# Kernel tuning notes

Hardware: AMD Instinct MI355X
Metric: run time of the kernel (lower is better)

Reference implementation:

```python
import jax, jax.numpy as jnp
import numpy as np

HEADS = 16
PHI = (1.0 + np.sqrt(5.0)) / 2.0


def setup_inputs() -> dict:
    key = jax.random.key(0)
    k1, k2, k3, k4 = jax.random.split(key, 4)
    B, L, D = 2, 2048, 1024
    x = jax.random.normal(k1, (B, L, D), dtype=jnp.float32)
    # nn.Linear(dim, 3*dim, bias=False): store as [D, 3D] for x @ W
    w_qkv = jax.random.normal(k2, (D, 3 * D), dtype=jnp.float32) * (D ** -0.5)
    w_proj = jax.random.normal(k3, (D, D), dtype=jnp.float32) * (D ** -0.5)
    b_proj = jax.random.normal(k4, (D,), dtype=jnp.float32) * 0.01
    return {"x": x, "w_qkv": w_qkv, "w_proj": w_proj, "b_proj": b_proj}


def phi_bias(L):
    # pos[i] = (i * phi) mod 1 ; bias = log(exp(-|pos_i - pos_j|) + 1e-8)
    pos = (jnp.arange(L, dtype=jnp.float32) * PHI) % 1.0
    dist = jnp.abs(pos[:, None] - pos[None, :])  # [L, L]
    return jnp.log(jnp.exp(-dist) + 1e-8)


def reference(x, w_qkv, w_proj, b_proj):
    B, L, D = x.shape
    H = HEADS
    Dh = D // H
    scale = Dh ** -0.5
    qkv = (x @ w_qkv).reshape(B, L, 3, H, Dh)
    q = jnp.transpose(qkv[:, :, 0], (0, 2, 1, 3))  # [B, H, L, Dh]
    k = jnp.transpose(qkv[:, :, 1], (0, 2, 1, 3))
    v = jnp.transpose(qkv[:, :, 2], (0, 2, 1, 3))
    attn = jnp.einsum("bhid,bhjd->bhij", q, k) * scale  # [B, H, L, L]
    attn = attn + phi_bias(L)[None, None]  # additive phi-distance bias
    attn = jax.nn.softmax(attn, axis=-1)
    out = jnp.einsum("bhij,bhjd->bhid", attn, v)  # [B, H, L, Dh]
    out = jnp.transpose(out, (0, 2, 1, 3)).reshape(B, L, D)
    return out @ w_proj + b_proj
```

## Files before the change

### kernel.cpp

```cpp
#include <hip/hip_runtime.h>
#include <math.h>


typedef _Float16 f16;
typedef _Float16 f16x4 __attribute__((ext_vector_type(4)));
typedef _Float16 f16x8 __attribute__((ext_vector_type(8)));
typedef float f32x4 __attribute__((ext_vector_type(4)));

#define MFMA32(a, b, c) __builtin_amdgcn_mfma_f32_16x16x32_f16(a, b, c, 0, 0, 0)

static constexpr int Bsz = 2, Lseq = 2048, Dm = 1024, H = 16, Dh = 64;
static constexpr int Mtot = Bsz * Lseq;
static constexpr int NQKV = 3 * Dm;
static constexpr float PHI_F = 1.61803398874989484820f;
static constexpr float LOG2E = 1.44269504088896f;
static constexpr float QS = 0.125f * LOG2E;
static constexpr float CSTEP = 0.55417527999932633f;

__device__ __forceinline__ void load16_to_lds(const f16* g, f16* l) {
  __builtin_amdgcn_global_load_lds(
      (const __attribute__((address_space(1))) unsigned int*)g,
      (__attribute__((address_space(3))) unsigned int*)l, 16, 0, 0);
}

__device__ __forceinline__ void barrier_fenced() {
  __builtin_amdgcn_sched_barrier(0);
  __builtin_amdgcn_s_barrier();
  __builtin_amdgcn_sched_barrier(0);
}

__global__ __launch_bounds__(256) void prep_fused(
    const float* __restrict__ x, f16* __restrict__ xb,
    const float* __restrict__ wqkv, f16* __restrict__ wqkvT,
    const float* __restrict__ wproj, f16* __restrict__ wpT) {
  __shared__ float tile[32][33];
  int blk = blockIdx.x;
  if (blk < 4096) {
    int i = (blk * 256 + threadIdx.x) * 4;
    float4 v = *reinterpret_cast<const float4*>(x + i);
    f16 t[4] = {(f16)v.x, (f16)v.y, (f16)v.z, (f16)v.w};
    *reinterpret_cast<uint2*>(xb + i) = *reinterpret_cast<uint2*>(t);
    return;
  }
  const float* in;
  f16* out;
  int N, bx, by;
  if (blk < 7168) {
    int local = blk - 4096;
    bx = local % 96; by = local / 96; N = NQKV;
    in = wqkv; out = wqkvT;
  } else {
    int local = blk - 7168;
    bx = local & 31; by = local >> 5; N = Dm;
    in = wproj; out = wpT;
  }
  int n0 = bx * 32, k0 = by * 32;
  int tx = threadIdx.x & 31, ty = threadIdx.x >> 5;
#pragma unroll
  for (int r = 0; r < 32; r += 8)
    tile[ty + r][tx] = in[(size_t)(k0 + ty + r) * N + n0 + tx];
  __syncthreads();
#pragma unroll
  for (int r = 0; r < 32; r += 8)
    out[(size_t)(n0 + ty + r) * Dm + k0 + tx] = (f16)tile[tx][ty + r];
}

__global__ __launch_bounds__(512, 1) void gemm_qkv(
    const f16* __restrict__ A, const f16* __restrict__ Bt,
    f16* __restrict__ qb, f16* __restrict__ kb, f16* __restrict__ vb) {
  __shared__ f16 As[2 * 256 * 64];
  __shared__ f16 Bs[2 * 192 * 64];

  int tid = threadIdx.x;
  int wave = tid >> 6, lane = tid & 63;
  int quad = lane >> 4, l16 = lane & 15;
  int warp_m = wave >> 2, warp_n = wave & 3;
  int wm = warp_m * 128, wn = warp_n * 48;

  int lid = blockIdx.x;
  int xcd = lid & 7, t = lid >> 3;
  int mg = xcd & 3, ng = xcd >> 2;
  int m0 = (mg * 4 + (t >> 3)) * 256;
  int n0 = (ng * 8 + (t & 7)) * 192;

  const int gu = (lane & 7) ^ (lane >> 3);
  const f16* gAb = A + (size_t)(m0 + wave * 8 + (lane >> 3)) * Dm + gu * 8;
  const f16* gBb = Bt + (size_t)(n0 + wave * 8 + (lane >> 3)) * Dm + gu * 8;

  auto stageA = [&](int buf, int h, int kn) __attribute__((always_inline)) {
#pragma unroll
    for (int i = 0; i < 2; i++)
      load16_to_lds(gAb + (size_t)(h * 128 + i * 64) * Dm + kn,
                    As + buf * 16384 + (h * 128 + i * 64 + wave * 8) * 64);
  };
  auto stageB = [&](int buf, int part, int kn) __attribute__((always_inline)) {
    if (part == 0) {
#pragma unroll
      for (int i = 0; i < 2; i++)
        load16_to_lds(gBb + (size_t)(i * 64) * Dm + kn,
                      Bs + buf * 12288 + (i * 64 + wave * 8) * 64);
    } else {
      load16_to_lds(gBb + (size_t)128 * Dm + kn,
                    Bs + buf * 12288 + (128 + wave * 8) * 64);
    }
  };

  f32x4 acc[8][3] = {};

  auto do_tile = [&](int buf, int t_) __attribute__((always_inline)) {
    const f16* Ab = As + buf * 16384 + (wm + l16) * 64;
    const f16* Bb = Bs + buf * 12288 + (wn + l16) * 64;
    int nbuf = buf ^ 1;
    int kA = ((t_ + 1) & 15) * 64;
    int kB = ((t_ + 2) & 15) * 64;

    f16x8 a[4][2], b0[2][2], b1[2];

#pragma unroll
    for (int m = 0; m < 4; m++)
#pragma unroll
      for (int s = 0; s < 2; s++)
        a[m][s] = *reinterpret_cast<const f16x8*>(
            Ab + m * 16 * 64 + (((s * 4 + quad) ^ (l16 & 7)) * 8));
#pragma unroll
    for (int n = 0; n < 2; n++)
#pragma unroll
      for (int s = 0; s < 2; s++)
        b0[n][s] = *reinterpret_cast<const f16x8*>(
            Bb + n * 16 * 64 + (((s * 4 + quad) ^ (l16 & 7)) * 8));
    stageA(nbuf, 0, kA);
    barrier_fenced();
    asm volatile("s_waitcnt lgkmcnt(0)" ::: "memory");
    __builtin_amdgcn_sched_barrier(0);
    __builtin_amdgcn_s_setprio(1);
#pragma unroll
    for (int m = 0; m < 4; m++)
#pragma unroll
      for (int n = 0; n < 2; n++) {
        acc[m][n] = MFMA32(a[m][0], b0[n][0], acc[m][n]);
        acc[m][n] = MFMA32(a[m][1], b0[n][1], acc[m][n]);
      }
    __builtin_amdgcn_s_setprio(0);
    barrier_fenced();

#pragma unroll
    for (int s = 0; s < 2; s++)
      b1[s] = *reinterpret_cast<const f16x8*>(
          Bb + 2 * 16 * 64 + (((s * 4 + quad) ^ (l16 & 7)) * 8));
    stageA(nbuf, 1, kA);
    barrier_fenced();
    asm volatile("s_waitcnt lgkmcnt(0)" ::: "memory");
    __builtin_amdgcn_sched_barrier(0);
    __builtin_amdgcn_s_setprio(1);
#pragma unroll
    for (int m = 0; m < 4; m++) {
      acc[m][2] = MFMA32(a[m][0], b1[0], acc[m][2]);
      acc[m][2] = MFMA32(a[m][1], b1[1], acc[m][2]);
    }
    __builtin_amdgcn_s_setprio(0);
    barrier_fenced();

#pragma unroll
    for (int m = 0; m < 4; m++)
#pragma unroll
      for (int s = 0; s < 2; s++)
        a[m][s] = *reinterpret_cast<const f16x8*>(
            Ab + (4 + m) * 16 * 64 + (((s * 4 + quad) ^ (l16 & 7)) * 8));
    stageB(buf, 0, kB);
    barrier_fenced();
    asm volatile("s_waitcnt lgkmcnt(0)" ::: "memory");
    __builtin_amdgcn_sched_barrier(0);
    __builtin_amdgcn_s_setprio(1);
#pragma unroll
    for (int m = 0; m < 4; m++)
#pragma unroll
      for (int n = 0; n < 2; n++) {
        acc[4 + m][n] = MFMA32(a[m][0], b0[n][0], acc[4 + m][n]);
        acc[4 + m][n] = MFMA32(a[m][1], b0[n][1], acc[4 + m][n]);
      }
    __builtin_amdgcn_s_setprio(0);
    barrier_fenced();

    stageB(buf, 1, kB);
    asm volatile("s_waitcnt vmcnt(3)" ::: "memory");
    barrier_fenced();
    __builtin_amdgcn_s_setprio(1);
#pragma unroll
    for (int m = 0; m < 4; m++) {
      acc[4 + m][2] = MFMA32(a[m][0], b1[0], acc[4 + m][2]);
      acc[4 + m][2] = MFMA32(a[m][1], b1[1], acc[4 + m][2]);
    }
    __builtin_amdgcn_s_setprio(0);
    barrier_fenced();
  };

  stageA(0, 0, 0);
  stageA(0, 1, 0);
  stageB(0, 0, 0);
  stageB(0, 1, 0);
  stageB(1, 0, 64);
  stageB(1, 1, 64);
  asm volatile("s_waitcnt vmcnt(3)" ::: "memory");
  barrier_fenced();

#pragma unroll 1
  for (int tt = 0; tt < 16; tt += 2) {
    do_tile(0, tt);
    do_tile(1, tt + 1);
  }
  asm volatile("s_waitcnt vmcnt(0)" ::: "memory");

#pragma unroll
  for (int i = 0; i < 8; i++) {
#pragma unroll
    for (int j = 0; j < 3; j++) {
      int n = n0 + wn + j * 16 + l16;
      int ty = n >> 10;
      int df = n & 1023;
      int h = df >> 6, dh = df & 63;
      int mb = m0 + wm + i * 16 + quad * 4;
      int b = mb >> 11, l = mb & 2047;
      int bhh = b * H + h;
      if (ty == 2) {
        int jj = l & 63;
        int jh = jj >> 5, rem = jj & 31;
        int qd = (rem & 15) >> 2;
        int e0 = (rem >= 16) ? 4 : 0;
        f16x4 tmp;
#pragma unroll
        for (int r = 0; r < 4; r++) tmp[r] = (f16)acc[i][j][r];
        *reinterpret_cast<uint2*>(
            vb + (size_t)bhh * (Dh * Lseq) + (l >> 6) * 4096 + dh * 64 +
            (jh * 4 + qd) * 8 + e0) = *reinterpret_cast<uint2*>(&tmp);
      } else {
        size_t idx = (((size_t)bhh) * Lseq + l) * Dh + dh;
        if (ty == 0) {
#pragma unroll
          for (int r = 0; r < 4; r++)
            qb[idx + (size_t)r * Dh] = (f16)(acc[i][j][r] * QS);
        } else {
#pragma unroll
          for (int r = 0; r < 4; r++)
            kb[idx + (size_t)r * Dh] = (f16)acc[i][j][r];
        }
      }
    }
  }
}

__global__ __launch_bounds__(256) void gemm_proj(
    const f16* __restrict__ A, const f16* __restrict__ Bt,
    float* __restrict__ out, const float* __restrict__ bias) {
  constexpr int MI = 4, AI = 4;
  __shared__ f16 As[2 * 128 * 64];
  __shared__ f16 Bs[2 * 128 * 64];

  int tid = threadIdx.x;
  int wave = tid >> 6, lane = tid & 63;
  int quad = lane >> 4, l16 = lane & 15;
  int wm = (wave >> 1) * 64, wn = (wave & 1) * 64;

  int lid = blockIdx.x;
  int xcd = lid & 7, t = lid >> 3;
  int m0 = (xcd * 4 + (t >> 3)) * 128;
  int n0 = (t & 7) * 128;

  const int gu = (lane & 7) ^ (lane >> 3);
  const f16* gA[AI];
  f16* lA[AI];
#pragma unroll
  for (int i = 0; i < AI; i++) {
    int it = wave * AI + i;
    gA[i] = A + (size_t)(m0 + it * 8 + (lane >> 3)) * Dm + gu * 8;
    lA[i] = As + it * 512;
  }
  const f16* gB[4];
  f16* lB[4];
#pragma unroll
  for (int i = 0; i < 4; i++) {
    int it = wave * 4 + i;
    gB[i] = Bt + (size_t)(n0 + it * 8 + (lane >> 3)) * Dm + gu * 8;
    lB[i] = Bs + it * 512;
  }

  auto stage = [&](int buf, int k0) __attribute__((always_inline)) {
#pragma unroll
    for (int i = 0; i < AI; i++) load16_to_lds(gA[i] + k0, lA[i] + buf * 8192);
#pragma unroll
    for (int i = 0; i < 4; i++) load16_to_lds(gB[i] + k0, lB[i] + buf * 8192);
  };

  f32x4 acc[MI][4] = {};

  stage(0, 0);
  asm volatile("s_waitcnt vmcnt(0)" ::: "memory");
  barrier_fenced();

#pragma unroll 1
  for (int kt = 0; kt < 16; kt++) {
    int buf = kt & 1;
    const f16* Ab = As + buf * 8192;
    const f16* Bb = Bs + buf * 8192;

    f16x8 a[2][MI], b[2][4];
#pragma unroll
    for (int s = 0; s < 2; s++) {
#pragma unroll
      for (int i = 0; i < MI; i++) {
        int row = wm + i * 16 + l16;
        a[s][i] = *reinterpret_cast<const f16x8*>(
            Ab + row * 64 + (((s * 4 + quad) ^ (l16 & 7)) * 8));
      }
#pragma unroll
      for (int j = 0; j < 4; j++) {
        int row = wn + j * 16 + l16;
        b[s][j] = *reinterpret_cast<const f16x8*>(
            Bb + row * 64 + (((s * 4 + quad) ^ (l16 & 7)) * 8));
      }
    }

    int kn = (kt + 1 < 16) ? (kt + 1) * 64 : 0;
    stage(buf ^ 1, kn);

    __builtin_amdgcn_s_setprio(1);
#pragma unroll
    for (int s = 0; s < 2; s++)
#pragma unroll
      for (int i = 0; i < MI; i++)
#pragma unroll
        for (int j = 0; j < 4; j++)
          acc[i][j] = MFMA32(a[s][i], b[s][j], acc[i][j]);
    __builtin_amdgcn_s_setprio(0);

    asm volatile("s_waitcnt vmcnt(0)" ::: "memory");
    barrier_fenced();
  }

#pragma unroll
  for (int i = 0; i < MI; i++)
#pragma unroll
    for (int j = 0; j < 4; j++) {
      int n = n0 + wn + j * 16 + l16;
#pragma unroll
      for (int r = 0; r < 4; r++) {
        int m = m0 + wm + i * 16 + quad * 4 + r;
        out[(size_t)m * Dm + n] = acc[i][j][r] + bias[n];
      }
    }
}

__global__ __launch_bounds__(512, 4) void attn_kernel(
    const f16* __restrict__ qb,
    const f16* __restrict__ kb,
    const f16* __restrict__ vb,
    f16* __restrict__ ctx) {
  __shared__ __align__(16) unsigned char smem[33280];
  f16* Ks = (f16*)smem;
  f16* Vs = (f16*)(smem + 8192);

  int id = blockIdx.x;
  int bh = (id & 7) * 4 + ((id >> 3) >> 4);
  int q0 = ((id >> 3) & 15) * 128;

  int tid = threadIdx.x, wave = tid >> 6, lane = tid & 63;
  int quad = lane >> 4, l16 = lane & 15;
  int jhalf = wave >> 2, qq = wave & 3;

  f16x8 qfrag[2][2];
  float pq[2];
#pragma unroll
  for (int set = 0; set < 2; set++) {
    int q = q0 + qq * 32 + set * 16 + l16;
    const f16* Qrow = qb + ((size_t)bh * Lseq + q) * Dh;
    qfrag[set][0] = *reinterpret_cast<const f16x8*>(Qrow + quad * 8);
    qfrag[set][1] = *reinterpret_cast<const f16x8*>(Qrow + 32 + quad * 8);
    pq[set] = fmodf((float)q * PHI_F, 1.0f);
  }

  float pk[2][4];
#pragma unroll
  for (int jb = 0; jb < 2; jb++)
#pragma unroll
    for (int r = 0; r < 4; r++) {
      int j = jhalf * 32 + jb * 16 + quad * 4 + r;
      pk[jb][r] = fmodf((float)j * PHI_F, 1.0f);
    }

  const f16* Kbh = kb + (size_t)bh * Lseq * Dh;
  const f16* Vbh = vb + (size_t)bh * Dh * Lseq;
  const int gu = (lane & 7) ^ (lane >> 3);
  int g8 = wave * 8 + (lane >> 3);
  const f16* gK = Kbh + (size_t)g8 * Dh + gu * 8;
  const f16* gV = Vbh + (size_t)g8 * 64 + gu * 8;
  f16* lK = Ks + wave * 512;
  f16* lV = Vs + wave * 512;

  const f16 one = (f16)1.0f;
  const f16x8 ones8 = {one, one, one, one, one, one, one, one};

  f32x4 acc_o[2][4] = {};
  f32x4 acc_l[2] = {};

  for (int j0 = 0; j0 < Lseq; j0 += 64) {
    __syncthreads();
    load16_to_lds(gK + (size_t)j0 * Dh, lK);
    load16_to_lds(gV + (size_t)j0 * 64, lV);
    __syncthreads();

    f32x4 accs[2][2] = {};
    __builtin_amdgcn_s_setprio(1);
#pragma unroll
    for (int s = 0; s < 2; s++)
#pragma unroll
      for (int jb = 0; jb < 2; jb++) {
        f16x8 kf = *reinterpret_cast<const f16x8*>(
            Ks + (jhalf * 32 + jb * 16 + l16) * 64 + (((s * 4 + quad) ^ (l16 & 7)) * 8));
        accs[0][jb] = MFMA32(kf, qfrag[0][s], accs[0][jb]);
        accs[1][jb] = MFMA32(kf, qfrag[1][s], accs[1][jb]);
      }
    __builtin_amdgcn_s_setprio(0);

    f16x8 pf8[2];
#pragma unroll
    for (int set = 0; set < 2; set++) {
#pragma unroll
      for (int jb = 0; jb < 2; jb++) {
        float p[4];
#pragma unroll
        for (int r = 0; r < 4; r++) {
          float d = pq[set] - pk[jb][r];
          float arg = fmaf(-LOG2E, fabsf(d), accs[set][jb][r]);
          p[r] = __builtin_amdgcn_exp2f(arg);
        }
        auto lo = __builtin_amdgcn_cvt_pkrtz(p[0], p[1]);
        auto hi = __builtin_amdgcn_cvt_pkrtz(p[2], p[3]);
        pf8[set][jb * 4 + 0] = lo[0];
        pf8[set][jb * 4 + 1] = lo[1];
        pf8[set][jb * 4 + 2] = hi[0];
        pf8[set][jb * 4 + 3] = hi[1];
      }
      acc_l[set] = MFMA32(ones8, pf8[set], acc_l[set]);
    }
#pragma unroll
    for (int jb = 0; jb < 2; jb++)
#pragma unroll
      for (int r = 0; r < 4; r++)
        pk[jb][r] = __builtin_amdgcn_fractf(pk[jb][r] + CSTEP);

    __builtin_amdgcn_s_setprio(1);
#pragma unroll
    for (int dblk = 0; dblk < 4; dblk++) {
      int row = dblk * 16 + l16;
      f16x8 va = *reinterpret_cast<const f16x8*>(
          Vs + row * 64 + (((jhalf * 4 + quad) ^ (l16 & 7)) * 8));
      acc_o[0][dblk] = MFMA32(va, pf8[0], acc_o[0][dblk]);
      acc_o[1][dblk] = MFMA32(va, pf8[1], acc_o[1][dblk]);
    }
    __builtin_amdgcn_s_setprio(0);
  }

  __syncthreads();
  float* Oex = (float*)smem;
  float* Lex = (float*)(smem + 32768);
  if (jhalf == 1) {
#pragma unroll
    for (int set = 0; set < 2; set++) {
#pragma unroll
      for (int dblk = 0; dblk < 4; dblk++)
#pragma unroll
        for (int r = 0; r < 4; r++)
          Oex[(((qq * 2 + set) * 4 + dblk) * 16 + quad * 4 + r) * 16 + l16] =
              acc_o[set][dblk][r];
      if (quad == 0) Lex[(qq * 2 + set) * 16 + l16] = acc_l[set][0];
    }
  }
  __syncthreads();
  if (jhalf == 0) {
    int b = bh >> 4, h = bh & 15;
#pragma unroll
    for (int set = 0; set < 2; set++) {
      float ltot = acc_l[set][0] + Lex[(qq * 2 + set) * 16 + l16];
      float inv = 1.0f / ltot;
      int q = q0 + qq * 32 + set * 16 + l16;
      f16* crow = ctx + (size_t)(b * Lseq + q) * Dm + h * 64;
#pragma unroll
      for (int dblk = 0; dblk < 4; dblk++) {
        f16x4 o;
#pragma unroll
        for (int r = 0; r < 4; r++) {
          float full = acc_o[set][dblk][r] +
              Oex[(((qq * 2 + set) * 4 + dblk) * 16 + quad * 4 + r) * 16 + l16];
          o[r] = (f16)(full * inv);
        }
        *reinterpret_cast<uint2*>(crow + dblk * 16 + quad * 4) =
            *reinterpret_cast<uint2*>(&o);
      }
    }
  }
}

extern "C" void kernel_launch(void* const* d_in, const int* in_sizes, int n_in,
                              void* d_out, int out_size, void* d_ws, size_t ws_size,
                              hipStream_t stream) {
  const float* x      = (const float*)d_in[0];
  const float* w_qkv  = (const float*)d_in[1];
  const float* w_proj = (const float*)d_in[2];
  const float* b_proj = (const float*)d_in[3];
  float* out = (float*)d_out;

  f16* xb    = (f16*)d_ws;
  f16* wqkvT = xb + (size_t)Mtot * Dm;
  f16* wpT   = wqkvT + (size_t)NQKV * Dm;
  f16* qb    = wpT + (size_t)Dm * Dm;
  f16* kb    = qb + (size_t)Bsz * H * Lseq * Dh;
  f16* vb    = kb + (size_t)Bsz * H * Lseq * Dh;
  f16* ctx   = vb + (size_t)Bsz * H * Lseq * Dh;

  prep_fused<<<8192, 256, 0, stream>>>(x, xb, w_qkv, wqkvT, w_proj, wpT);

  gemm_qkv<<<256, 512, 0, stream>>>(xb, wqkvT, qb, kb, vb);

  attn_kernel<<<512, 512, 0, stream>>>(qb, kb, vb, ctx);

  gemm_proj<<<256, 256, 0, stream>>>(ctx, wpT, out, b_proj);
}
```

Measured before the change: 173.0 us.

## Double-buffer K/V tiles in LDS to overlap global loads with attention compute

```diff
diff --git a/kernel.cpp b/kernel.cpp
--- a/kernel.cpp
+++ b/kernel.cpp
@@ -356,7 +356,7 @@
     f16* __restrict__ ctx) {
   __shared__ __align__(16) unsigned char smem[33280];
   f16* Ks = (f16*)smem;
-  f16* Vs = (f16*)(smem + 8192);
+  f16* Vs = (f16*)(smem + 16384);
 
   int id = blockIdx.x;
   int bh = (id & 7) * 4 + ((id >> 3) >> 4);
@@ -395,17 +395,44 @@
   f16* lK = Ks + wave * 512;
   f16* lV = Vs + wave * 512;
 
+  auto stage = [&](int buf, int j0) __attribute__((always_inline)) {
+    load16_to_lds(gK + (size_t)j0 * Dh, lK + buf * 4096);
+    load16_to_lds(gV + (size_t)j0 * 64, lV + buf * 4096);
+  };
+
   const f16 one = (f16)1.0f;
   const f16x8 ones8 = {one, one, one, one, one, one, one, one};
 
   f32x4 acc_o[2][4] = {};
   f32x4 acc_l[2] = {};
 
+  const f16* Kfb = Ks + (jhalf * 32 + l16) * 64;
+  const f16* Vfb = Vs + l16 * 64 + (((jhalf * 4 + quad) ^ (l16 & 7)) * 8);
+
+  stage(0, 0);
+  asm volatile("s_waitcnt vmcnt(0)" ::: "memory");
+  barrier_fenced();
+
+#pragma unroll 1
   for (int j0 = 0; j0 < Lseq; j0 += 64) {
-    __syncthreads();
-    load16_to_lds(gK + (size_t)j0 * Dh, lK);
-    load16_to_lds(gV + (size_t)j0 * 64, lV);
-    __syncthreads();
+    int buf = (j0 >> 6) & 1;
+    const f16* Kc = Kfb + buf * 4096;
+    const f16* Vc = Vfb + buf * 4096;
+
+    f16x8 kf[2][2];
+#pragma unroll
+    for (int s = 0; s < 2; s++)
+#pragma unroll
+      for (int jb = 0; jb < 2; jb++)
+        kf[s][jb] = *reinterpret_cast<const f16x8*>(
+            Kc + jb * 16 * 64 + (((s * 4 + quad) ^ (l16 & 7)) * 8));
+    f16x8 va[4];
+#pragma unroll
+    for (int dblk = 0; dblk < 4; dblk++)
+      va[dblk] = *reinterpret_cast<const f16x8*>(Vc + dblk * 16 * 64);
+
+    int jn = (j0 + 64 < Lseq) ? j0 + 64 : 0;
+    stage(buf ^ 1, jn);
 
     f32x4 accs[2][2] = {};
     __builtin_amdgcn_s_setprio(1);
@@ -413,10 +440,8 @@
     for (int s = 0; s < 2; s++)
 #pragma unroll
       for (int jb = 0; jb < 2; jb++) {
-        f16x8 kf = *reinterpret_cast<const f16x8*>(
-            Ks + (jhalf * 32 + jb * 16 + l16) * 64 + (((s * 4 + quad) ^ (l16 & 7)) * 8));
-        accs[0][jb] = MFMA32(kf, qfrag[0][s], accs[0][jb]);
-        accs[1][jb] = MFMA32(kf, qfrag[1][s], accs[1][jb]);
+        accs[0][jb] = MFMA32(kf[s][jb], qfrag[0][s], accs[0][jb]);
+        accs[1][jb] = MFMA32(kf[s][jb], qfrag[1][s], accs[1][jb]);
       }
     __builtin_amdgcn_s_setprio(0);
 
@@ -450,16 +475,15 @@
     __builtin_amdgcn_s_setprio(1);
 #pragma unroll
     for (int dblk = 0; dblk < 4; dblk++) {
-      int row = dblk * 16 + l16;
-      f16x8 va = *reinterpret_cast<const f16x8*>(
-          Vs + row * 64 + (((jhalf * 4 + quad) ^ (l16 & 7)) * 8));
-      acc_o[0][dblk] = MFMA32(va, pf8[0], acc_o[0][dblk]);
-      acc_o[1][dblk] = MFMA32(va, pf8[1], acc_o[1][dblk]);
-    }
-    __builtin_amdgcn_s_setprio(0);
-  }
-
-  __syncthreads();
+      acc_o[0][dblk] = MFMA32(va[dblk], pf8[0], acc_o[0][dblk]);
+      acc_o[1][dblk] = MFMA32(va[dblk], pf8[1], acc_o[1][dblk]);
+    }
+    __builtin_amdgcn_s_setprio(0);
+
+    asm volatile("s_waitcnt vmcnt(0)" ::: "memory");
+    barrier_fenced();
+  }
+
   float* Oex = (float*)smem;
   float* Lex = (float*)(smem + 32768);
   if (jhalf == 1) {
```

After: 173.6 us. About the same (+0.3%).
